# Optimization experiments

Measured on AMD Instinct MI355X. Metric: run time of the kernel, lower is better.

Reference implementation:

```python
import jax, jax.numpy as jnp
import numpy as np

B, T, D_MODEL = 4, 4096, 1024
H = 16
DH = D_MODEL // H
EPS = 1e-6
CHUNK = 128


def _feature(x):
    # elu(x) + 1
    return jnp.where(x > 0, x + 1.0, jnp.exp(x))


def _causal_dot_product(Q, K, V):
    """Q,K,V: [B,H,T,D]. out[t] = Q[t] @ sum_{s<=t} K[s]^T V[s]. Chunked scan, O(T*D^2)."""
    b, h, t, d = Q.shape
    nc = t // CHUNK
    mask = jnp.tril(jnp.ones((CHUNK, CHUNK), dtype=Q.dtype))
    # [NC, B, H, C, D]
    qs = jnp.moveaxis(Q.reshape(b, h, nc, CHUNK, d), 2, 0)
    ks = jnp.moveaxis(K.reshape(b, h, nc, CHUNK, d), 2, 0)
    vs = jnp.moveaxis(V.reshape(b, h, nc, CHUNK, d), 2, 0)

    def step(S, qkv):
        q, k, v = qkv  # each [B,H,C,D]
        attn = jnp.einsum('bhid,bhjd->bhij', q, k) * mask  # intra-chunk causal
        out = jnp.einsum('bhij,bhjd->bhid', attn, v) + jnp.einsum('bhid,bhde->bhie', q, S)
        S = S + jnp.einsum('bhcd,bhce->bhde', k, v)
        return S, out

    S0 = jnp.zeros((b, h, d, d), dtype=Q.dtype)
    _, outs = jax.lax.scan(step, S0, (qs, ks, vs))
    return jnp.moveaxis(outs, 0, 2).reshape(b, h, t, d)


def setup_inputs() -> dict:
    key = jax.random.key(0)
    ks = jax.random.split(key, 6)
    s = 0.02
    x = jax.random.normal(ks[0], (B, T, D_MODEL), dtype=jnp.float32)
    Wq = jax.random.normal(ks[1], (D_MODEL, D_MODEL), dtype=jnp.float32) * s
    Wk = jax.random.normal(ks[2], (D_MODEL, D_MODEL), dtype=jnp.float32) * s
    Wv = jax.random.normal(ks[3], (D_MODEL, D_MODEL), dtype=jnp.float32) * s
    Wo = jax.random.normal(ks[4], (D_MODEL, D_MODEL), dtype=jnp.float32) * s
    bo = jax.random.normal(ks[5], (D_MODEL,), dtype=jnp.float32) * s
    return {"x": x, "Wq": Wq, "Wk": Wk, "Wv": Wv, "Wo": Wo, "bo": bo}


def reference(x, Wq, Wk, Wv, Wo, bo):
    b, t, _ = x.shape
    def proj(W):
        return (x @ W).reshape(b, t, H, DH).transpose(0, 2, 1, 3)  # [B,H,T,Dh]
    Q = _feature(proj(Wq))
    K = _feature(proj(Wk))
    V = proj(Wv)
    # Faithful to source: cumsum over axis 1 of the [B,H,T,D] layout (head axis)
    Z = 1.0 / (jnp.einsum('bhtd,bhtd->bht', Q, jnp.cumsum(K, axis=1)) + EPS)
    unnorm = _causal_dot_product(Q, K, V)
    out = unnorm * Z[..., None]  # [B,H,T,Dh]
    out = out.transpose(0, 2, 1, 3).reshape(b, t, H * DH)
    return out @ Wo + bo  # dropout is identity in eval
```

## Files before the change

kernel.cpp:

```cpp
#include <hip/hip_runtime.h>
#include <hip/hip_bf16.h>

#define BATCH 4
#define SEQ   4096
#define DMODEL 1024
#define NH    16
#define DH    64
#define NCHUNK 32
#define CHUNKSZ 128
#define FEPS  1e-6f

typedef unsigned short ushort_t;
typedef __attribute__((ext_vector_type(8))) short short8;
typedef __attribute__((ext_vector_type(4))) float f32x4;
typedef __attribute__((ext_vector_type(16))) float f32x16;

__device__ __forceinline__ float bf2f(ushort_t u) {
    union { unsigned int i; float f; } x; x.i = ((unsigned int)u) << 16; return x.f;
}
__device__ __forceinline__ ushort_t f2bf(float f) {
    union { float f; unsigned int i; } x; x.f = f;
    unsigned int lsb = (x.i >> 16) & 1u;
    x.i += 0x7fffu + lsb;
    return (ushort_t)(x.i >> 16);
}

__device__ __forceinline__ void load_lds16(const void* g, void* l) {
    __builtin_amdgcn_global_load_lds(
        (const __attribute__((address_space(1))) int*)g,
        (__attribute__((address_space(3))) int*)l, 16, 0, 0);
}

__global__ __launch_bounds__(256) void prep_k(const float* __restrict__ X,
                                              ushort_t* __restrict__ Xb,
                                              const float* __restrict__ W0,
                                              const float* __restrict__ W1,
                                              const float* __restrict__ W2,
                                              const float* __restrict__ W3,
                                              ushort_t* __restrict__ WT0)
{
    __shared__ float tile[32][33];
    const int id = blockIdx.x;
    const int tid = threadIdx.x;
    if (id < 4096) {
        const float* Ws[4] = {W0, W1, W2, W3};
        const int wz = id >> 10, rem = id & 1023;
        const float* W = Ws[wz];
        ushort_t* WT = WT0 + (size_t)wz * DMODEL * DMODEL;
        int tx = tid & 31, ty = tid >> 5;
        int kb = (rem & 31) << 5, nb = (rem >> 5) << 5;
#pragma unroll
        for (int i = 0; i < 4; i++)
            tile[ty + i * 8][tx] = W[(size_t)(kb + ty + i * 8) * DMODEL + nb + tx];
        __syncthreads();
#pragma unroll
        for (int i = 0; i < 4; i++)
            WT[(size_t)(nb + ty + i * 8) * DMODEL + kb + tx] = f2bf(tile[tx][ty + i * 8]);
    } else {
        const int n4 = (int)((size_t)BATCH * SEQ * DMODEL / 4);
        int i = (id - 4096) * 256 + tid;
        const int stride = 2048 * 256;
        for (; i < n4; i += stride) {
            float4 v = ((const float4*)X)[i];
            ushort4 u;
            u.x = f2bf(v.x); u.y = f2bf(v.y); u.z = f2bf(v.z); u.w = f2bf(v.w);
            ((ushort4*)Xb)[i] = u;
        }
    }
}

#define TBM 256
#define TBN 256
#define TBK 32

template<int MODE>
__global__ __launch_bounds__(512, 2) void mgemm32_k(const ushort_t* __restrict__ Ap,
                                                    const ushort_t* __restrict__ Bt,
                                                    const float* __restrict__ bias,
                                                    void* __restrict__ Cp,
                                                    int M, int N, int K)
{
    __shared__ short smem[65536];
    const int tid = threadIdx.x;
    const int l  = tid & 63;
    const int w  = tid >> 6;
    const int wm = w >> 2, wn = w & 3;
    const int l31 = l & 31;
    const int hi  = l >> 5;

    const size_t m0 = (size_t)blockIdx.x * TBM;
    const size_t n0 = (size_t)blockIdx.y * TBN;

    f32x16 acc[4][2];
#pragma unroll
    for (int i = 0; i < 4; i++)
#pragma unroll
        for (int j = 0; j < 2; j++)
#pragma unroll
            for (int e = 0; e < 16; e++) acc[i][j][e] = 0.f;

    auto STAGE_PAIR = [&](int slot, int k0, int i) {
        short* Asl = smem + slot * 16384;
        short* Bsl = Asl + 8192;
        const int sa  = w * 2 + i;
        const int kch = sa >> 2;
        const int rb  = sa & 3;
        const int ldso = (kch * 256 + rb * 64) * 8;
        load_lds16(Ap + (m0 + rb * 64 + l) * (size_t)K + k0 + kch * 8, Asl + ldso);
        load_lds16(Bt + (n0 + rb * 64 + l) * (size_t)K + k0 + kch * 8, Bsl + ldso);
    };

    const int nt = K / TBK;
    STAGE_PAIR(0, 0, 0);       STAGE_PAIR(0, 0, 1);
    STAGE_PAIR(1, TBK, 0);     STAGE_PAIR(1, TBK, 1);
    STAGE_PAIR(2, 2 * TBK, 0); STAGE_PAIR(2, 2 * TBK, 1);
    asm volatile("s_waitcnt vmcnt(8)" ::: "memory");
    __builtin_amdgcn_sched_barrier(0);
    __builtin_amdgcn_s_barrier();

    for (int t = 0; t < nt; ++t) {
        const short* Asl = smem + (t & 3) * 16384;
        const short* Bsl = Asl + 8192;
        const bool pre = (t + 3 < nt);
        const int pslot = (t + 3) & 3;
        const int pk0 = (t + 3) * TBK;

        if (pre) STAGE_PAIR(pslot, pk0, 0);
        short8 a0[4], b0[2];
#pragma unroll
        for (int mt = 0; mt < 4; mt++)
            a0[mt] = *(const short8*)(Asl + (hi * 256 + wm * 128 + mt * 32 + l31) * 8);
#pragma unroll
        for (int nn = 0; nn < 2; nn++)
            b0[nn] = *(const short8*)(Bsl + (hi * 256 + wn * 64 + nn * 32 + l31) * 8);
        __builtin_amdgcn_sched_barrier(0);
        __builtin_amdgcn_s_barrier();
        asm volatile("s_waitcnt lgkmcnt(0)" ::: "memory");
        __builtin_amdgcn_sched_barrier(0);
        __builtin_amdgcn_s_setprio(1);
#pragma unroll
        for (int mt = 0; mt < 4; mt++)
#pragma unroll
            for (int nn = 0; nn < 2; nn++)
                acc[mt][nn] = __builtin_amdgcn_mfma_f32_32x32x16_bf16(
                    a0[mt], b0[nn], acc[mt][nn], 0, 0, 0);
        __builtin_amdgcn_s_setprio(0);
        __builtin_amdgcn_s_barrier();

        if (pre) STAGE_PAIR(pslot, pk0, 1);
        short8 a1[4], b1[2];
#pragma unroll
        for (int mt = 0; mt < 4; mt++)
            a1[mt] = *(const short8*)(Asl + ((2 + hi) * 256 + wm * 128 + mt * 32 + l31) * 8);
#pragma unroll
        for (int nn = 0; nn < 2; nn++)
            b1[nn] = *(const short8*)(Bsl + ((2 + hi) * 256 + wn * 64 + nn * 32 + l31) * 8);
        __builtin_amdgcn_sched_barrier(0);
        __builtin_amdgcn_s_barrier();
        asm volatile("s_waitcnt lgkmcnt(0)" ::: "memory");
        __builtin_amdgcn_sched_barrier(0);
        __builtin_amdgcn_s_setprio(1);
#pragma unroll
        for (int mt = 0; mt < 4; mt++)
#pragma unroll
            for (int nn = 0; nn < 2; nn++)
                acc[mt][nn] = __builtin_amdgcn_mfma_f32_32x32x16_bf16(
                    a1[mt], b1[nn], acc[mt][nn], 0, 0, 0);
        __builtin_amdgcn_s_setprio(0);

        if (t + 3 < nt) {
            asm volatile("s_waitcnt vmcnt(8)" ::: "memory");
        } else if (t + 2 < nt) {
            asm volatile("s_waitcnt vmcnt(4)" ::: "memory");
        } else if (t + 1 < nt) {
            asm volatile("s_waitcnt vmcnt(0)" ::: "memory");
        }
        __builtin_amdgcn_sched_barrier(0);
        __builtin_amdgcn_s_barrier();
    }

#pragma unroll
    for (int mt = 0; mt < 4; mt++) {
#pragma unroll
        for (int nn = 0; nn < 2; nn++) {
#pragma unroll
            for (int reg = 0; reg < 16; reg++) {
                int row = (reg & 3) + 8 * (reg >> 2) + 4 * hi;
                int m = (int)m0 + wm * 128 + mt * 32 + row;
                int n = (int)n0 + wn * 64 + nn * 32 + l31;
                float v = acc[mt][nn][reg];
                if (MODE == 2) {
                    ((float*)Cp)[(size_t)m * N + n] = v + bias[n];
                } else {
                    if (n < 2048) v = (v > 0.f) ? (v + 1.f) : __expf(v);
                    int tns = n >> 10, nnn = n & 1023;
                    int b_ = m >> 12, t_ = m & 4095, h_ = nnn >> 6, d_ = nnn & 63;
                    ushort_t* base = (ushort_t*)Cp + (size_t)tns * BATCH * SEQ * DMODEL;
                    base[((((size_t)b_ * NH + h_) * SEQ + t_) << 6) + d_] = f2bf(v);
                }
            }
        }
    }
}

__global__ __launch_bounds__(256) void zkv_k(const ushort_t* __restrict__ Qf,
                                             const ushort_t* __restrict__ Kf,
                                             const ushort_t* __restrict__ Vf,
                                             float* __restrict__ Z,
                                             ushort_t* __restrict__ Sloc)
{
    __shared__ short KTs[8192];
    __shared__ short VTs[8192];
    const int id = blockIdx.x;
    const int tid = threadIdx.x;
    if (id < 4096) {
        int bt = id * 4 + (tid >> 6);
        int b_ = bt >> 12, t_ = bt & 4095;
        int d = tid & 63;
        float qv[NH], kv[NH];
        size_t base = (((size_t)b_ * NH) * SEQ + t_) * DH + d;
#pragma unroll
        for (int h = 0; h < NH; h++) {
            qv[h] = bf2f(Qf[base + (size_t)h * SEQ * DH]);
            kv[h] = bf2f(Kf[base + (size_t)h * SEQ * DH]);
        }
        float ck = 0.f;
#pragma unroll
        for (int h = 0; h < NH; h++) {
            ck += kv[h];
            float p = qv[h] * ck;
#pragma unroll
            for (int off = 1; off < 64; off <<= 1) p += __shfl_xor(p, off, 64);
            if (d == 0) Z[((size_t)b_ * NH + h) * SEQ + t_] = 1.f / (p + FEPS);
        }
        return;
    }
    const int blk = id - 4096;
    const int l = tid & 63, w = tid >> 6;
    const int lr = l & 15, hi = l >> 4;
    const size_t rowbase = ((size_t)(blk >> 5) * SEQ + (size_t)(blk & 31) * CHUNKSZ) * DH;
    const uint4* K16 = (const uint4*)(Kf + rowbase);
    const uint4* V16 = (const uint4*)(Vf + rowbase);
#pragma unroll
    for (int i = 0; i < 4; i++) {
        int idx = tid + i * 256;
        union { uint4 q; ushort_t us[8]; } kk, vv;
        kk.q = K16[idx]; vv.q = V16[idx];
        int j = idx >> 3, e0 = (idx & 7) << 3;
#pragma unroll
        for (int s = 0; s < 8; s++) {
            int off = ((j >> 3) * 64 + e0 + s) * 8 + (j & 7);
            KTs[off] = (short)kk.us[s];
            VTs[off] = (short)vv.us[s];
        }
    }
    __syncthreads();
    f32x4 acc[4];
#pragma unroll
    for (int nt = 0; nt < 4; nt++) acc[nt] = (f32x4){0.f, 0.f, 0.f, 0.f};
#pragma unroll
    for (int ks = 0; ks < 4; ks++) {
        short8 af = *(const short8*)(KTs + ((ks * 4 + hi) * 64 + w * 16 + lr) * 8);
        short8 bf[4];
#pragma unroll
        for (int nt = 0; nt < 4; nt++)
            bf[nt] = *(const short8*)(VTs + ((ks * 4 + hi) * 64 + nt * 16 + lr) * 8);
#pragma unroll
        for (int nt = 0; nt < 4; nt++)
            acc[nt] = __builtin_amdgcn_mfma_f32_16x16x32_bf16(af, bf[nt], acc[nt], 0, 0, 0);
    }
    ushort_t* outp = Sloc + (size_t)blk * DH * DH;
#pragma unroll
    for (int nt = 0; nt < 4; nt++)
#pragma unroll
        for (int jr = 0; jr < 4; jr++) {
            int d_ = w * 16 + hi * 4 + jr;
            int e_ = nt * 16 + lr;
            outp[d_ * DH + e_] = f2bf(acc[nt][jr]);
        }
}

__global__ __launch_bounds__(256) void scan_k(ushort_t* __restrict__ Sloc)
{
    int bh = blockIdx.x, seg = blockIdx.y;
    int e = seg * 256 + threadIdx.x;
    ushort_t* base = Sloc + (size_t)bh * NCHUNK * DH * DH + e;
    float v[NCHUNK];
#pragma unroll
    for (int cc = 0; cc < NCHUNK; cc++) v[cc] = bf2f(base[(size_t)cc * DH * DH]);
    float acc = 0.f;
#pragma unroll
    for (int cc = 0; cc < NCHUNK; cc++) {
        float t = v[cc];
        base[(size_t)cc * DH * DH] = f2bf(acc);
        acc += t;
    }
}

__global__ __launch_bounds__(256) void attn_k(const ushort_t* __restrict__ Qf,
                                              const ushort_t* __restrict__ Kf,
                                              const ushort_t* __restrict__ Vf,
                                              const ushort_t* __restrict__ Sloc,
                                              const float* __restrict__ Z,
                                              ushort_t* __restrict__ A)
{
    __shared__ short smem[36864];
    short* Qs  = smem;
    short* Ks  = smem + 8192;
    short* Ps  = smem + 8192;
    short* VTs = smem + 24576;
    short* STs = smem + 32768;

    const int tid = threadIdx.x;
    const int l = tid & 63, w = tid >> 6;
    const int lr = l & 15, hi = l >> 4;
    const int blk = blockIdx.x;
    const int c = blk & (NCHUNK - 1), bh = blk >> 5;
    const int b_ = bh >> 4, h_ = bh & 15;
    const size_t rowbase = ((size_t)bh * SEQ + (size_t)c * CHUNKSZ) * DH;

#pragma unroll
    for (int ii = 0; ii < 4; ii++) {
        int s = w * 4 + ii;
        int kc2 = s >> 1, rh = (s & 1) << 6;
        int ldso = (kc2 * 128 + rh) * 8;
        load_lds16(Qf + rowbase + (size_t)(rh + l) * DH + kc2 * 8, Qs + ldso);
        load_lds16(Kf + rowbase + (size_t)(rh + l) * DH + kc2 * 8, Ks + ldso);
    }
    {
        const uint4* V16 = (const uint4*)(Vf + rowbase);
#pragma unroll
        for (int i = 0; i < 4; i++) {
            int idx = tid + i * 256;
            union { uint4 q; ushort_t us[8]; } vv;
            vv.q = V16[idx];
            int j = idx >> 3, e0 = (idx & 7) << 3;
#pragma unroll
            for (int s = 0; s < 8; s++)
                VTs[((j >> 3) * 64 + e0 + s) * 8 + (j & 7)] = (short)vv.us[s];
        }
    }
    {
        const uint4* S16 = (const uint4*)(Sloc + (size_t)blk * DH * DH);
#pragma unroll
        for (int i = 0; i < 2; i++) {
            int idx = tid + i * 256;
            union { uint4 q; ushort_t us[8]; } ss;
            ss.q = S16[idx];
            int d = idx >> 3, e0 = (idx & 7) << 3;
#pragma unroll
            for (int s = 0; s < 8; s++)
                STs[((d >> 3) * 64 + e0 + s) * 8 + (d & 7)] = (short)ss.us[s];
        }
    }
    __syncthreads();

    f32x4 acc1[2][8];
#pragma unroll
    for (int mt = 0; mt < 2; mt++)
#pragma unroll
        for (int nt = 0; nt < 8; nt++) acc1[mt][nt] = (f32x4){0.f, 0.f, 0.f, 0.f};
#pragma unroll
    for (int ks = 0; ks < 2; ks++) {
        short8 af[2], bf[8];
#pragma unroll
        for (int mt = 0; mt < 2; mt++)
            af[mt] = *(const short8*)(Qs + ((ks * 4 + hi) * 128 + w * 32 + mt * 16 + lr) * 8);
#pragma unroll
        for (int nt = 0; nt < 8; nt++)
            bf[nt] = *(const short8*)(Ks + ((ks * 4 + hi) * 128 + nt * 16 + lr) * 8);
#pragma unroll
        for (int mt = 0; mt < 2; mt++)
#pragma unroll
            for (int nt = 0; nt < 8; nt++)
                acc1[mt][nt] = __builtin_amdgcn_mfma_f32_16x16x32_bf16(
                    af[mt], bf[nt], acc1[mt][nt], 0, 0, 0);
    }
    __syncthreads();

#pragma unroll
    for (int mt = 0; mt < 2; mt++)
#pragma unroll
        for (int nt = 0; nt < 8; nt++)
#pragma unroll
            for (int jr = 0; jr < 4; jr++) {
                int i_ = w * 32 + mt * 16 + hi * 4 + jr;
                int j_ = nt * 16 + lr;
                float v = (j_ <= i_) ? acc1[mt][nt][jr] : 0.f;
                Ps[((j_ >> 3) * 128 + i_) * 8 + (j_ & 7)] = (short)f2bf(v);
            }
    __syncthreads();

    f32x4 acc2[2][4];
#pragma unroll
    for (int mt = 0; mt < 2; mt++)
#pragma unroll
        for (int nt = 0; nt < 4; nt++) acc2[mt][nt] = (f32x4){0.f, 0.f, 0.f, 0.f};
#pragma unroll
    for (int ks = 0; ks < 4; ks++) {
        short8 af[2], bf[4];
#pragma unroll
        for (int mt = 0; mt < 2; mt++)
            af[mt] = *(const short8*)(Ps + ((ks * 4 + hi) * 128 + w * 32 + mt * 16 + lr) * 8);
#pragma unroll
        for (int nt = 0; nt < 4; nt++)
            bf[nt] = *(const short8*)(VTs + ((ks * 4 + hi) * 64 + nt * 16 + lr) * 8);
#pragma unroll
        for (int mt = 0; mt < 2; mt++)
#pragma unroll
            for (int nt = 0; nt < 4; nt++)
                acc2[mt][nt] = __builtin_amdgcn_mfma_f32_16x16x32_bf16(
                    af[mt], bf[nt], acc2[mt][nt], 0, 0, 0);
    }
#pragma unroll
    for (int ks = 0; ks < 2; ks++) {
        short8 af[2], bf[4];
#pragma unroll
        for (int mt = 0; mt < 2; mt++)
            af[mt] = *(const short8*)(Qs + ((ks * 4 + hi) * 128 + w * 32 + mt * 16 + lr) * 8);
#pragma unroll
        for (int nt = 0; nt < 4; nt++)
            bf[nt] = *(const short8*)(STs + ((ks * 4 + hi) * 64 + nt * 16 + lr) * 8);
#pragma unroll
        for (int mt = 0; mt < 2; mt++)
#pragma unroll
            for (int nt = 0; nt < 4; nt++)
                acc2[mt][nt] = __builtin_amdgcn_mfma_f32_16x16x32_bf16(
                    af[mt], bf[nt], acc2[mt][nt], 0, 0, 0);
    }

#pragma unroll
    for (int mt = 0; mt < 2; mt++) {
#pragma unroll
        for (int jr = 0; jr < 4; jr++) {
            int i_ = w * 32 + mt * 16 + hi * 4 + jr;
            int t_ = c * CHUNKSZ + i_;
            float z = Z[(size_t)bh * SEQ + t_];
            ushort_t* op = A + (((size_t)(b_ * SEQ + t_)) * NH + h_) * DH;
#pragma unroll
            for (int nt = 0; nt < 4; nt++)
                op[nt * 16 + lr] = f2bf(acc2[mt][nt][jr] * z);
        }
    }
}

extern "C" void kernel_launch(void* const* d_in, const int* in_sizes, int n_in,
                              void* d_out, int out_size, void* d_ws, size_t ws_size,
                              hipStream_t stream)
{
    const float* x  = (const float*)d_in[0];
    const float* Wq = (const float*)d_in[1];
    const float* Wk = (const float*)d_in[2];
    const float* Wv = (const float*)d_in[3];
    const float* Wo = (const float*)d_in[4];
    const float* bo = (const float*)d_in[5];
    float* out = (float*)d_out;

    const size_t NEL = (size_t)BATCH * SEQ * DMODEL;
    const size_t WEL = (size_t)DMODEL * DMODEL;
    ushort_t* Qb  = (ushort_t*)d_ws;
    ushort_t* Kb  = Qb + NEL;
    ushort_t* Vb  = Kb + NEL;
    ushort_t* XAb = Vb + NEL;
    float*    Zb  = (float*)(XAb + NEL);
    ushort_t* WTq = (ushort_t*)(Zb + (size_t)BATCH * NH * SEQ);
    ushort_t* WTo = WTq + 3 * WEL;
    ushort_t* Sl  = (ushort_t*)d_out;

    const int M = BATCH * SEQ;

    prep_k<<<dim3(6144), dim3(256), 0, stream>>>(x, XAb, Wq, Wk, Wv, Wo, WTq);

    mgemm32_k<0><<<dim3(M / TBM, 3 * DMODEL / TBN), dim3(512), 0, stream>>>(
        XAb, WTq, nullptr, Qb, M, 3 * DMODEL, DMODEL);

    zkv_k<<<dim3(6144), dim3(256), 0, stream>>>(Qb, Kb, Vb, Zb, Sl);

    scan_k<<<dim3(BATCH * NH, 16), dim3(256), 0, stream>>>(Sl);
    attn_k<<<dim3(BATCH * NH * NCHUNK), dim3(256), 0, stream>>>(Qb, Kb, Vb, Sl, Zb, XAb);

    mgemm32_k<2><<<dim3(M / TBM, DMODEL / TBN), dim3(512), 0, stream>>>(
        XAb, WTo, bo, out, M, DMODEL, DMODEL);
}
```

Baseline: 285.4 us.

## Restructure GEMM to TBK=64 double-buffered pipeline with per-phase prefetch

The bf16 MFMA GEMM used for the QKV and output projections now uses a K-tile of 64 instead of 32. The 4-slot, 3-deep prefetch ring becomes a 2-buffer double-buffer, and each of the four k-subgroups issues its global-to-LDS load for the next tile interleaved with the MFMAs. This is meant to halve loop iterations and barrier overhead and give more MFMA work per sync. In exchange it reduces prefetch depth to one tile ahead, which may expose memory latency, and the vmcnt accounting must be right for correctness.

Measured after the change: 396.6 us. +39.0%, slower.

```diff
diff --git a/kernel.cpp b/kernel.cpp
--- a/kernel.cpp
+++ b/kernel.cpp
@@ -71,10 +71,36 @@
 
 #define TBM 256
 #define TBN 256
-#define TBK 32
+#define TBK 64
+
+#define MPHASE(GG, VM, DOSTAGE)                                               \
+    {                                                                         \
+        short8 a_[4], b_[2];                                                  \
+        _Pragma("unroll")                                                     \
+        for (int mt = 0; mt < 4; mt++)                                        \
+            a_[mt] = *(const short8*)(buf + ((2*(GG)+hi)*256 + wm*128 + mt*32 + l31)*8); \
+        _Pragma("unroll")                                                     \
+        for (int nn = 0; nn < 2; nn++)                                        \
+            b_[nn] = *(const short8*)(buf + 16384 + ((2*(GG)+hi)*256 + wn*64 + nn*32 + l31)*8); \
+        if (DOSTAGE) STAGE(nbuf, pk0, GG);                                    \
+        __builtin_amdgcn_sched_barrier(0);                                    \
+        asm volatile("s_waitcnt vmcnt(" VM ")" ::: "memory");                 \
+        __builtin_amdgcn_sched_barrier(0);                                    \
+        __builtin_amdgcn_s_barrier();                                         \
+        asm volatile("s_waitcnt lgkmcnt(0)" ::: "memory");                    \
+        __builtin_amdgcn_sched_barrier(0);                                    \
+        __builtin_amdgcn_s_setprio(1);                                        \
+        _Pragma("unroll")                                                     \
+        for (int mt = 0; mt < 4; mt++)                                        \
+            _Pragma("unroll")                                                 \
+            for (int nn = 0; nn < 2; nn++)                                    \
+                acc[mt][nn] = __builtin_amdgcn_mfma_f32_32x32x16_bf16(        \
+                    a_[mt], b_[nn], acc[mt][nn], 0, 0, 0);                    \
+        __builtin_amdgcn_s_setprio(0);                                        \
+    }
 
 template<int MODE>
-__global__ __launch_bounds__(512, 2) void mgemm32_k(const ushort_t* __restrict__ Ap,
+__global__ __launch_bounds__(512, 2) void mgemm64_k(const ushort_t* __restrict__ Ap,
                                                     const ushort_t* __restrict__ Bt,
                                                     const float* __restrict__ bias,
                                                     void* __restrict__ Cp,
@@ -99,84 +125,38 @@
 #pragma unroll
             for (int e = 0; e < 16; e++) acc[i][j][e] = 0.f;
 
-    auto STAGE_PAIR = [&](int slot, int k0, int i) {
-        short* Asl = smem + slot * 16384;
-        short* Bsl = Asl + 8192;
-        const int sa  = w * 2 + i;
-        const int kch = sa >> 2;
-        const int rb  = sa & 3;
-        const int ldso = (kch * 256 + rb * 64) * 8;
-        load_lds16(Ap + (m0 + rb * 64 + l) * (size_t)K + k0 + kch * 8, Asl + ldso);
-        load_lds16(Bt + (n0 + rb * 64 + l) * (size_t)K + k0 + kch * 8, Bsl + ldso);
+    auto STAGE = [&](short* dst, int k0, int g) {
+        const int kc  = g * 2 + (tid >> 8);
+        const int row = tid & 255;
+        load_lds16(Ap + (m0 + row) * (size_t)K + k0 + kc * 8, dst + g * 4096 + tid * 8);
+        load_lds16(Bt + (n0 + row) * (size_t)K + k0 + kc * 8, dst + 16384 + g * 4096 + tid * 8);
     };
 
     const int nt = K / TBK;
-    STAGE_PAIR(0, 0, 0);       STAGE_PAIR(0, 0, 1);
-    STAGE_PAIR(1, TBK, 0);     STAGE_PAIR(1, TBK, 1);
-    STAGE_PAIR(2, 2 * TBK, 0); STAGE_PAIR(2, 2 * TBK, 1);
-    asm volatile("s_waitcnt vmcnt(8)" ::: "memory");
+    STAGE(smem, 0, 0); STAGE(smem, 0, 1); STAGE(smem, 0, 2); STAGE(smem, 0, 3);
+    asm volatile("s_waitcnt vmcnt(6)" ::: "memory");
     __builtin_amdgcn_sched_barrier(0);
     __builtin_amdgcn_s_barrier();
 
-    for (int t = 0; t < nt; ++t) {
-        const short* Asl = smem + (t & 3) * 16384;
-        const short* Bsl = Asl + 8192;
-        const bool pre = (t + 3 < nt);
-        const int pslot = (t + 3) & 3;
-        const int pk0 = (t + 3) * TBK;
-
-        if (pre) STAGE_PAIR(pslot, pk0, 0);
-        short8 a0[4], b0[2];
-#pragma unroll
-        for (int mt = 0; mt < 4; mt++)
-            a0[mt] = *(const short8*)(Asl + (hi * 256 + wm * 128 + mt * 32 + l31) * 8);
-#pragma unroll
-        for (int nn = 0; nn < 2; nn++)
-            b0[nn] = *(const short8*)(Bsl + (hi * 256 + wn * 64 + nn * 32 + l31) * 8);
+    for (int t = 0; t < nt - 1; ++t) {
+        short* buf  = smem + (t & 1) * 32768;
+        short* nbuf = smem + ((t & 1) ^ 1) * 32768;
+        const int pk0 = (t + 1) * TBK;
+        MPHASE(0, "6", true)
+        MPHASE(1, "6", true)
+        MPHASE(2, "6", true)
+        MPHASE(3, "6", true)
         __builtin_amdgcn_sched_barrier(0);
         __builtin_amdgcn_s_barrier();
-        asm volatile("s_waitcnt lgkmcnt(0)" ::: "memory");
-        __builtin_amdgcn_sched_barrier(0);
-        __builtin_amdgcn_s_setprio(1);
-#pragma unroll
-        for (int mt = 0; mt < 4; mt++)
-#pragma unroll
-            for (int nn = 0; nn < 2; nn++)
-                acc[mt][nn] = __builtin_amdgcn_mfma_f32_32x32x16_bf16(
-                    a0[mt], b0[nn], acc[mt][nn], 0, 0, 0);
-        __builtin_amdgcn_s_setprio(0);
-        __builtin_amdgcn_s_barrier();
-
-        if (pre) STAGE_PAIR(pslot, pk0, 1);
-        short8 a1[4], b1[2];
-#pragma unroll
-        for (int mt = 0; mt < 4; mt++)
-            a1[mt] = *(const short8*)(Asl + ((2 + hi) * 256 + wm * 128 + mt * 32 + l31) * 8);
-#pragma unroll
-        for (int nn = 0; nn < 2; nn++)
-            b1[nn] = *(const short8*)(Bsl + ((2 + hi) * 256 + wn * 64 + nn * 32 + l31) * 8);
-        __builtin_amdgcn_sched_barrier(0);
-        __builtin_amdgcn_s_barrier();
-        asm volatile("s_waitcnt lgkmcnt(0)" ::: "memory");
-        __builtin_amdgcn_sched_barrier(0);
-        __builtin_amdgcn_s_setprio(1);
-#pragma unroll
-        for (int mt = 0; mt < 4; mt++)
-#pragma unroll
-            for (int nn = 0; nn < 2; nn++)
-                acc[mt][nn] = __builtin_amdgcn_mfma_f32_32x32x16_bf16(
-                    a1[mt], b1[nn], acc[mt][nn], 0, 0, 0);
-        __builtin_amdgcn_s_setprio(0);
-
-        if (t + 3 < nt) {
-            asm volatile("s_waitcnt vmcnt(8)" ::: "memory");
-        } else if (t + 2 < nt) {
-            asm volatile("s_waitcnt vmcnt(4)" ::: "memory");
-        } else if (t + 1 < nt) {
-            asm volatile("s_waitcnt vmcnt(0)" ::: "memory");
-        }
-        __builtin_amdgcn_sched_barrier(0);
-        __builtin_amdgcn_s_barrier();
+    }
+    {
+        short* buf  = smem + ((nt - 1) & 1) * 32768;
+        short* nbuf = buf;  (void)nbuf;
+        const int pk0 = 0;  (void)pk0;
+        MPHASE(0, "4", false)
+        MPHASE(1, "2", false)
+        MPHASE(2, "0", false)
+        MPHASE(3, "0", false)
     }
 
 #pragma unroll
@@ -471,7 +451,7 @@
 
     prep_k<<<dim3(6144), dim3(256), 0, stream>>>(x, XAb, Wq, Wk, Wv, Wo, WTq);
 
-    mgemm32_k<0><<<dim3(M / TBM, 3 * DMODEL / TBN), dim3(512), 0, stream>>>(
+    mgemm64_k<0><<<dim3(M / TBM, 3 * DMODEL / TBN), dim3(512), 0, stream>>>(
         XAb, WTq, nullptr, Qb, M, 3 * DMODEL, DMODEL);
 
     zkv_k<<<dim3(6144), dim3(256), 0, stream>>>(Qb, Kb, Vb, Zb, Sl);
@@ -479,6 +459,6 @@
     scan_k<<<dim3(BATCH * NH, 16), dim3(256), 0, stream>>>(Sl);
     attn_k<<<dim3(BATCH * NH * NCHUNK), dim3(256), 0, stream>>>(Qb, Kb, Vb, Sl, Zb, XAb);
 
-    mgemm32_k<2><<<dim3(M / TBM, DMODEL / TBN), dim3(512), 0, stream>>>(
+    mgemm64_k<2><<<dim3(M / TBM, DMODEL / TBN), dim3(512), 0, stream>>>(
         XAb, WTo, bo, out, M, DMODEL, DMODEL);
 }
```
